# Kernel optimization log

Measured on AMD Instinct MI355X. Metric: run time of the kernel, lower is better.

Reference implementation:

```python
import jax, jax.numpy as jnp
import numpy as np

IN_SIZES = [64, 128, 256]
HIDDEN = [512, 512]
ENC = 256
COUNTS = [100000, 80000, 60000]


def _xavier(key, fan_in, fan_out):
    # xavier_uniform with gain('sigmoid') == 1
    lim = float(np.sqrt(6.0 / (fan_in + fan_out)))
    return jax.random.uniform(key, (fan_in, fan_out), jnp.float32, -lim, lim)


def setup_inputs() -> dict:
    key = jax.random.key(0)
    ks = jax.random.split(key, 32)
    inp = {}
    ki = 0
    for t, (n, d) in enumerate(zip(COUNTS, IN_SIZES)):
        inp[f"x{t}"] = jax.random.normal(ks[ki], (n, d), dtype=jnp.float32)
        ki += 1
    # node_type sorted by type, counts match x tensors (invariant of the module)
    inp["node_type"] = jnp.concatenate(
        [jnp.full((n,), t, dtype=jnp.int32) for t, n in enumerate(COUNTS)])
    for t, d_in in enumerate(IN_SIZES):
        sizes = [d_in] + HIDDEN + [ENC]
        for i in range(len(sizes) - 1):
            inp[f"W{t}_{i+1}"] = _xavier(ks[ki], sizes[i], sizes[i + 1])
            ki += 1
            inp[f"b{t}_{i+1}"] = jnp.zeros((sizes[i + 1],), jnp.float32)
    return inp


def _mlp(x, layers):
    # each layer is Linear followed by Sigmoid (including the last)
    for W, b in layers:
        x = jax.nn.sigmoid(x @ W + b)
    return x


def reference(x0, x1, x2, node_type,
              W0_1, b0_1, W0_2, b0_2, W0_3, b0_3,
              W1_1, b1_1, W1_2, b1_2, W1_3, b1_3,
              W2_1, b2_1, W2_2, b2_2, W2_3, b2_3):
    xs = [x0, x1, x2]
    params = [
        [(W0_1, b0_1), (W0_2, b0_2), (W0_3, b0_3)],
        [(W1_1, b1_1), (W1_2, b1_2), (W1_3, b1_3)],
        [(W2_1, b2_1), (W2_2, b2_2), (W2_3, b2_3)],
    ]
    N = node_type.shape[0]
    X = jnp.zeros((N, ENC), dtype=jnp.float32)
    for nt in range(len(xs)):
        # static per-type count -> fixed-size nonzero works under jit
        idx = jnp.nonzero(node_type == nt, size=xs[nt].shape[0])[0]
        X = X.at[idx].set(_mlp(xs[nt], params[nt]))
    return X
```

## Files before the change

kernel.cpp:

```cpp
#include <hip/hip_runtime.h>
#include <hip/hip_bf16.h>

typedef __bf16 bf16x8 __attribute__((ext_vector_type(8)));
typedef __bf16 bf16x4 __attribute__((ext_vector_type(4)));
typedef float  f32x16 __attribute__((ext_vector_type(16)));

#define MFMA __builtin_amdgcn_mfma_f32_32x32x16_bf16
#define BM 64
#define S  520
#define SF 260

struct PrepParams {
    const float* src[9];
    int Kt[9];
    int Mg[9];
    int N[9];
    int blkEnd[9];
    int unitBase[9];
};

__global__ void __launch_bounds__(256)
prep_weights(PrepParams p, uint4* __restrict__ dst) {
    __shared__ float tile[32][128];
    int b = blockIdx.x;
    int w = 0;
    while (b >= p.blkEnd[w]) ++w;
    int local = b - ((w == 0) ? 0 : p.blkEnd[w - 1]);
    int mgc = p.Mg[w];
    int kt = local / mgc;
    int mg = local - kt * mgc;
    const float* src = p.src[w];
    int N = p.N[w];
    int Kc = p.Kt[w] * 2;
    int t = threadIdx.x;

    int row0 = kt * 32, col0 = mg * 128;
#pragma unroll
    for (int i = 0; i < 4; ++i) {
        int e4 = t + i * 256;
        int r = e4 >> 5;
        int c4 = e4 & 31;
        float4 v = *(const float4*)&src[(size_t)(row0 + r) * N + col0 + c4 * 4];
        *(float4*)&tile[r][c4 * 4] = v;
    }
    __syncthreads();

#pragma unroll
    for (int rep = 0; rep < 2; ++rep) {
        int ul = t + rep * 256;
        int lane = ul & 63;
        int kcl = (ul >> 6) & 1;
        int mtl = ul >> 7;
        int gUnit = p.unitBase[w] +
                    ((mg * 4 + mtl) * Kc + (kt * 2 + kcl)) * 64 + lane;
        int lr = kcl * 16 + ((lane >> 5) << 3);
        int lc = mtl * 32 + (lane & 31);
        alignas(16) unsigned short u8[8];
#pragma unroll
        for (int j = 0; j < 8; ++j)
            u8[j] = __builtin_bit_cast(unsigned short, (__bf16)tile[lr + j][lc]);
        dst[gUnit] = *(const uint4*)u8;
    }
}

struct MlpParams {
    const float* X[3];
    const unsigned short* Wp[3];
    const float* B1[3];
    const float* B2[3];
    const float* B3[3];
    int dIn[3];
    int Nt[3];
    int rowOff[3];
};

__device__ __forceinline__ float sigmoidf(float z) {
    return __builtin_amdgcn_rcpf(
        1.0f + __builtin_amdgcn_exp2f(-1.442695040888963f * z));
}

template <int K16, int MT, bool TO_LDS>
__device__ __forceinline__ void layerP(
    unsigned short* __restrict__ buf,
    const unsigned short* __restrict__ W,
    const float* __restrict__ bias,
    int wave, int lane)
{
    const int half = lane >> 5;
    const int lr = lane & 31;

    f32x16 acc[2][MT];
#pragma unroll
    for (int n = 0; n < 2; ++n)
#pragma unroll
        for (int m = 0; m < MT; ++m)
#pragma unroll
            for (int e = 0; e < 16; ++e)
                acc[n][m][e] = 0.0f;

    const unsigned short* bp0 = buf + lr * S + half * 8;
    const unsigned short* bp1 = bp0 + 32 * S;
    const unsigned short* ap = W + (size_t)wave * MT * K16 * 512 + lane * 8;

    bf16x8 aPf[2][MT];
#pragma unroll
    for (int d = 0; d < 2; ++d)
#pragma unroll
        for (int m = 0; m < MT; ++m)
            aPf[d][m] = *(const bf16x8*)(ap + ((size_t)m * K16 + d) * 512);

#pragma unroll 1
    for (int kb = 0; kb + 3 < K16; kb += 2) {
#pragma unroll
        for (int u = 0; u < 2; ++u) {
            int k = kb + u;
            bf16x8 b0 = *(const bf16x8*)(bp0 + k * 16);
            bf16x8 b1 = *(const bf16x8*)(bp1 + k * 16);
            bf16x8 a[MT];
#pragma unroll
            for (int m = 0; m < MT; ++m) a[m] = aPf[u][m];
#pragma unroll
            for (int m = 0; m < MT; ++m)
                aPf[u][m] =
                    *(const bf16x8*)(ap + ((size_t)m * K16 + k + 2) * 512);
#pragma unroll
            for (int m = 0; m < MT; ++m) {
                acc[0][m] = MFMA(a[m], b0, acc[0][m], 0, 0, 0);
                acc[1][m] = MFMA(a[m], b1, acc[1][m], 0, 0, 0);
            }
        }
    }
#pragma unroll
    for (int u = 0; u < 2; ++u) {
        int k = K16 - 2 + u;
        bf16x8 b0 = *(const bf16x8*)(bp0 + k * 16);
        bf16x8 b1 = *(const bf16x8*)(bp1 + k * 16);
#pragma unroll
        for (int m = 0; m < MT; ++m) {
            acc[0][m] = MFMA(aPf[u][m], b0, acc[0][m], 0, 0, 0);
            acc[1][m] = MFMA(aPf[u][m], b1, acc[1][m], 0, 0, 0);
        }
    }

#pragma unroll
    for (int m = 0; m < MT; ++m) {
        int mt = wave * MT + m;
#pragma unroll
        for (int g = 0; g < 4; ++g) {
            int f0 = mt * 32 + g * 8 + half * 4;
            float4 bv = *(const float4*)(bias + f0);
#pragma unroll
            for (int n = 0; n < 2; ++n) {
                acc[n][m][g * 4 + 0] = sigmoidf(acc[n][m][g * 4 + 0] + bv.x);
                acc[n][m][g * 4 + 1] = sigmoidf(acc[n][m][g * 4 + 1] + bv.y);
                acc[n][m][g * 4 + 2] = sigmoidf(acc[n][m][g * 4 + 2] + bv.z);
                acc[n][m][g * 4 + 3] = sigmoidf(acc[n][m][g * 4 + 3] + bv.w);
            }
        }
    }

    __syncthreads();

#pragma unroll
    for (int m = 0; m < MT; ++m) {
        int mt = wave * MT + m;
#pragma unroll
        for (int g = 0; g < 4; ++g) {
            int f0 = mt * 32 + g * 8 + half * 4;
#pragma unroll
            for (int n = 0; n < 2; ++n) {
                int r = n * 32 + lr;
                if constexpr (TO_LDS) {
                    bf16x4 h = {(__bf16)acc[n][m][g * 4 + 0],
                                (__bf16)acc[n][m][g * 4 + 1],
                                (__bf16)acc[n][m][g * 4 + 2],
                                (__bf16)acc[n][m][g * 4 + 3]};
                    *(bf16x4*)(buf + r * S + f0) = h;
                } else {
                    float* fb = (float*)buf;
                    *(float4*)(fb + r * SF + f0) =
                        make_float4(acc[n][m][g * 4 + 0], acc[n][m][g * 4 + 1],
                                    acc[n][m][g * 4 + 2], acc[n][m][g * 4 + 3]);
                }
            }
        }
    }
}

__global__ void __launch_bounds__(512, 4)
mlp_fused(MlpParams p, float* __restrict__ out) {
    extern __shared__ unsigned short buf[];

    int g = blockIdx.x;
    int rep = g / 12;
    int pos = g - rep * 12;
    int t = (int)((0x186124u >> (pos * 2)) & 3u);
    int rk = (int)((0x8D3451200ULL >> (pos * 3)) & 7u);
    int blk = rep * (5 - t) + rk;

    int dIn = p.dIn[t];
    int Nt = p.Nt[t];
    int row0 = blk * BM;
    const float* X = p.X[t];
    const unsigned short* W1 = p.Wp[t];
    const unsigned short* W2 = W1 + dIn * 512;
    const unsigned short* W3 = W2 + 512 * 512;

    int tid = threadIdx.x;
    int wave = tid >> 6;
    int lane = tid & 63;

    int d4 = dIn >> 2;
    int s4 = 31 - __clz(d4);
    int nf4 = BM * d4;
    for (int i = tid; i < nf4; i += 512) {
        int r = i >> s4;
        int c4 = i & (d4 - 1);
        int grow = row0 + r;
        float4 v = make_float4(0.f, 0.f, 0.f, 0.f);
        if (grow < Nt) v = ((const float4*)X)[(size_t)grow * d4 + c4];
        ushort4 u;
        u.x = __builtin_bit_cast(unsigned short, (__bf16)v.x);
        u.y = __builtin_bit_cast(unsigned short, (__bf16)v.y);
        u.z = __builtin_bit_cast(unsigned short, (__bf16)v.z);
        u.w = __builtin_bit_cast(unsigned short, (__bf16)v.w);
        *(ushort4*)(buf + r * S + c4 * 4) = u;
    }
    __syncthreads();

    if (t == 0)      layerP<4,  2, true>(buf, W1, p.B1[0], wave, lane);
    else if (t == 1) layerP<8,  2, true>(buf, W1, p.B1[1], wave, lane);
    else             layerP<16, 2, true>(buf, W1, p.B1[2], wave, lane);
    __syncthreads();
    layerP<32, 2, true>(buf, W2, p.B2[t], wave, lane);
    __syncthreads();
    layerP<32, 1, false>(buf, W3, p.B3[t], wave, lane);
    __syncthreads();

    const float* fb = (const float*)buf;
    float* gOut = out + (size_t)(p.rowOff[t] + row0) * 256;
    for (int i = tid; i < BM * 64; i += 512) {
        int r = i >> 6;
        int c4 = i & 63;
        if (row0 + r < Nt)
            *(float4*)(gOut + r * 256 + c4 * 4) =
                *(const float4*)(fb + r * SF + c4 * 4);
    }
}

extern "C" void kernel_launch(void* const* d_in, const int* in_sizes, int n_in,
                              void* d_out, int out_size, void* d_ws, size_t ws_size,
                              hipStream_t stream) {
    const int IN0[3] = {64, 128, 256};
    const int CNT[3] = {100000, 80000, 60000};

    PrepParams pp;
    int blocks = 0, ubase = 0;
    for (int t = 0; t < 3; ++t) {
        int Ks[3] = {IN0[t], 512, 512};
        int Ns[3] = {512, 512, 256};
        for (int l = 0; l < 3; ++l) {
            int w = t * 3 + l;
            pp.src[w] = (const float*)d_in[4 + t * 6 + l * 2];
            pp.Kt[w] = Ks[l] >> 5;
            pp.Mg[w] = Ns[l] >> 7;
            pp.N[w] = Ns[l];
            pp.unitBase[w] = ubase;
            blocks += pp.Kt[w] * pp.Mg[w];
            pp.blkEnd[w] = blocks;
            ubase += (Ks[l] * Ns[l]) >> 3;
        }
    }
    prep_weights<<<dim3(blocks), dim3(256), 0, stream>>>(pp, (uint4*)d_ws);

    MlpParams mp;
    int woff = 0, roff = 0, boff = 0;
    for (int t = 0; t < 3; ++t) {
        mp.X[t] = (const float*)d_in[t];
        mp.Wp[t] = (const unsigned short*)d_ws + woff;
        mp.B1[t] = (const float*)d_in[4 + t * 6 + 1];
        mp.B2[t] = (const float*)d_in[4 + t * 6 + 3];
        mp.B3[t] = (const float*)d_in[4 + t * 6 + 5];
        mp.dIn[t] = IN0[t];
        mp.Nt[t] = CNT[t];
        mp.rowOff[t] = roff;
        woff += IN0[t] * 512 + 512 * 512 + 512 * 256;
        roff += CNT[t];
        boff += (CNT[t] + BM - 1) / BM;
    }
    size_t lds = (size_t)BM * S * sizeof(unsigned short);
    mlp_fused<<<dim3(boff), dim3(512), lds, stream>>>(mp, (float*)d_out);
}
```

Measured before the change: 559.6 us.

## Halve row tile to 32 with 4 waves each covering more output columns

```diff
diff --git a/kernel.cpp b/kernel.cpp
--- a/kernel.cpp
+++ b/kernel.cpp
@@ -6,7 +6,7 @@
 typedef float  f32x16 __attribute__((ext_vector_type(16)));
 
 #define MFMA __builtin_amdgcn_mfma_f32_32x32x16_bf16
-#define BM 64
+#define BM 32
 #define S  520
 #define SF 260
 
@@ -89,17 +89,14 @@
     const int half = lane >> 5;
     const int lr = lane & 31;
 
-    f32x16 acc[2][MT];
-#pragma unroll
-    for (int n = 0; n < 2; ++n)
-#pragma unroll
-        for (int m = 0; m < MT; ++m)
-#pragma unroll
-            for (int e = 0; e < 16; ++e)
-                acc[n][m][e] = 0.0f;
+    f32x16 acc[MT];
+#pragma unroll
+    for (int m = 0; m < MT; ++m)
+#pragma unroll
+        for (int e = 0; e < 16; ++e)
+            acc[m][e] = 0.0f;
 
     const unsigned short* bp0 = buf + lr * S + half * 8;
-    const unsigned short* bp1 = bp0 + 32 * S;
     const unsigned short* ap = W + (size_t)wave * MT * K16 * 512 + lane * 8;
 
     bf16x8 aPf[2][MT];
@@ -115,7 +112,6 @@
         for (int u = 0; u < 2; ++u) {
             int k = kb + u;
             bf16x8 b0 = *(const bf16x8*)(bp0 + k * 16);
-            bf16x8 b1 = *(const bf16x8*)(bp1 + k * 16);
             bf16x8 a[MT];
 #pragma unroll
             for (int m = 0; m < MT; ++m) a[m] = aPf[u][m];
@@ -124,22 +120,17 @@
                 aPf[u][m] =
                     *(const bf16x8*)(ap + ((size_t)m * K16 + k + 2) * 512);
 #pragma unroll
-            for (int m = 0; m < MT; ++m) {
-                acc[0][m] = MFMA(a[m], b0, acc[0][m], 0, 0, 0);
-                acc[1][m] = MFMA(a[m], b1, acc[1][m], 0, 0, 0);
-            }
+            for (int m = 0; m < MT; ++m)
+                acc[m] = MFMA(a[m], b0, acc[m], 0, 0, 0);
         }
     }
 #pragma unroll
     for (int u = 0; u < 2; ++u) {
         int k = K16 - 2 + u;
         bf16x8 b0 = *(const bf16x8*)(bp0 + k * 16);
-        bf16x8 b1 = *(const bf16x8*)(bp1 + k * 16);
-#pragma unroll
-        for (int m = 0; m < MT; ++m) {
-            acc[0][m] = MFMA(aPf[u][m], b0, acc[0][m], 0, 0, 0);
-            acc[1][m] = MFMA(aPf[u][m], b1, acc[1][m], 0, 0, 0);
-        }
+#pragma unroll
+        for (int m = 0; m < MT; ++m)
+            acc[m] = MFMA(aPf[u][m], b0, acc[m], 0, 0, 0);
     }
 
 #pragma unroll
@@ -149,13 +140,10 @@
         for (int g = 0; g < 4; ++g) {
             int f0 = mt * 32 + g * 8 + half * 4;
             float4 bv = *(const float4*)(bias + f0);
-#pragma unroll
-            for (int n = 0; n < 2; ++n) {
-                acc[n][m][g * 4 + 0] = sigmoidf(acc[n][m][g * 4 + 0] + bv.x);
-                acc[n][m][g * 4 + 1] = sigmoidf(acc[n][m][g * 4 + 1] + bv.y);
-                acc[n][m][g * 4 + 2] = sigmoidf(acc[n][m][g * 4 + 2] + bv.z);
-                acc[n][m][g * 4 + 3] = sigmoidf(acc[n][m][g * 4 + 3] + bv.w);
-            }
+            acc[m][g * 4 + 0] = sigmoidf(acc[m][g * 4 + 0] + bv.x);
+            acc[m][g * 4 + 1] = sigmoidf(acc[m][g * 4 + 1] + bv.y);
+            acc[m][g * 4 + 2] = sigmoidf(acc[m][g * 4 + 2] + bv.z);
+            acc[m][g * 4 + 3] = sigmoidf(acc[m][g * 4 + 3] + bv.w);
         }
     }
 
@@ -167,27 +155,24 @@
 #pragma unroll
         for (int g = 0; g < 4; ++g) {
             int f0 = mt * 32 + g * 8 + half * 4;
-#pragma unroll
-            for (int n = 0; n < 2; ++n) {
-                int r = n * 32 + lr;
-                if constexpr (TO_LDS) {
-                    bf16x4 h = {(__bf16)acc[n][m][g * 4 + 0],
-                                (__bf16)acc[n][m][g * 4 + 1],
-                                (__bf16)acc[n][m][g * 4 + 2],
-                                (__bf16)acc[n][m][g * 4 + 3]};
-                    *(bf16x4*)(buf + r * S + f0) = h;
-                } else {
-                    float* fb = (float*)buf;
-                    *(float4*)(fb + r * SF + f0) =
-                        make_float4(acc[n][m][g * 4 + 0], acc[n][m][g * 4 + 1],
-                                    acc[n][m][g * 4 + 2], acc[n][m][g * 4 + 3]);
-                }
+            int r = lr;
+            if constexpr (TO_LDS) {
+                bf16x4 h = {(__bf16)acc[m][g * 4 + 0],
+                            (__bf16)acc[m][g * 4 + 1],
+                            (__bf16)acc[m][g * 4 + 2],
+                            (__bf16)acc[m][g * 4 + 3]};
+                *(bf16x4*)(buf + r * S + f0) = h;
+            } else {
+                float* fb = (float*)buf;
+                *(float4*)(fb + r * SF + f0) =
+                    make_float4(acc[m][g * 4 + 0], acc[m][g * 4 + 1],
+                                acc[m][g * 4 + 2], acc[m][g * 4 + 3]);
             }
         }
     }
 }
 
-__global__ void __launch_bounds__(512, 4)
+__global__ void __launch_bounds__(256, 4)
 mlp_fused(MlpParams p, float* __restrict__ out) {
     extern __shared__ unsigned short buf[];
 
@@ -213,7 +198,7 @@
     int d4 = dIn >> 2;
     int s4 = 31 - __clz(d4);
     int nf4 = BM * d4;
-    for (int i = tid; i < nf4; i += 512) {
+    for (int i = tid; i < nf4; i += 256) {
         int r = i >> s4;
         int c4 = i & (d4 - 1);
         int grow = row0 + r;
@@ -228,18 +213,18 @@
     }
     __syncthreads();
 
-    if (t == 0)      layerP<4,  2, true>(buf, W1, p.B1[0], wave, lane);
-    else if (t == 1) layerP<8,  2, true>(buf, W1, p.B1[1], wave, lane);
-    else             layerP<16, 2, true>(buf, W1, p.B1[2], wave, lane);
-    __syncthreads();
-    layerP<32, 2, true>(buf, W2, p.B2[t], wave, lane);
-    __syncthreads();
-    layerP<32, 1, false>(buf, W3, p.B3[t], wave, lane);
+    if (t == 0)      layerP<4,  4, true>(buf, W1, p.B1[0], wave, lane);
+    else if (t == 1) layerP<8,  4, true>(buf, W1, p.B1[1], wave, lane);
+    else             layerP<16, 4, true>(buf, W1, p.B1[2], wave, lane);
+    __syncthreads();
+    layerP<32, 4, true>(buf, W2, p.B2[t], wave, lane);
+    __syncthreads();
+    layerP<32, 2, false>(buf, W3, p.B3[t], wave, lane);
     __syncthreads();
 
     const float* fb = (const float*)buf;
     float* gOut = out + (size_t)(p.rowOff[t] + row0) * 256;
-    for (int i = tid; i < BM * 64; i += 512) {
+    for (int i = tid; i < BM * 64; i += 256) {
         int r = i >> 6;
         int c4 = i & 63;
         if (row0 + r < Nt)
@@ -289,5 +274,5 @@
         boff += (CNT[t] + BM - 1) / BM;
     }
     size_t lds = (size_t)BM * S * sizeof(unsigned short);
-    mlp_fused<<<dim3(boff), dim3(512), lds, stream>>>(mp, (float*)d_out);
-}
+    mlp_fused<<<dim3(boff), dim3(256), lds, stream>>>(mp, (float*)d_out);
+}
```

New measurement: 650.9 us. 16.3% more time.
